# Performance work log

Measured on AMD Instinct MI355X. Metric: run time of the kernel, lower is better.

The kernel has to match this reference:

```python
import jax, jax.numpy as jnp
import numpy as np

B, S, D, H = 2, 2048, 1024, 16
DK = D // H
NEG = -1e9


def setup_inputs() -> dict:
    key = jax.random.key(0)
    ks = jax.random.split(key, 12)
    sc = 1.0 / np.sqrt(D)
    inp = {
        "query": jax.random.normal(ks[0], (B, S, D), jnp.float32),
        "key": jax.random.normal(ks[1], (B, S, D), jnp.float32),
        "value": jax.random.normal(ks[2], (B, S, D), jnp.float32),
        "mask": jnp.ones((B, 1, S), jnp.int32),
        "Wq": jax.random.normal(ks[3], (D, D), jnp.float32) * sc,
        "bq": jnp.zeros((D,), jnp.float32),
        "Wk": jax.random.normal(ks[4], (D, D), jnp.float32) * sc,
        "bk": jnp.zeros((D,), jnp.float32),
        "Wv": jax.random.normal(ks[5], (D, D), jnp.float32) * sc,
        "bv": jnp.zeros((D,), jnp.float32),
        "Wo": jax.random.normal(ks[6], (D, D), jnp.float32) * sc,
        "bo": jnp.zeros((D,), jnp.float32),
    }
    return inp


def reference(query, key, value, mask, Wq, bq, Wk, bk, Wv, bv, Wo, bo):
    # projections + split heads: [B,S,D] -> [B,H,S,DK]
    def proj(x, W, b):
        return (x @ W + b).reshape(B, S, H, DK).transpose(0, 2, 1, 3)

    q = proj(query, Wq, bq)
    k = proj(key, Wk, bk)
    v = proj(value, Wv, bv)

    scores = jnp.einsum("bhqd,bhkd->bhqk", q, k) / jnp.sqrt(jnp.float32(DK))
    # mask: [B,1,S] -> unsqueeze head dim -> [B,1,1,S], broadcast over heads & queries
    m = mask[:, None, :, :]  # [B,1,1,S]
    scores = jnp.where(m == 0, NEG, scores)
    p_attn = jax.nn.softmax(scores, axis=-1)  # dropout p=0 (eval)
    x = jnp.einsum("bhqk,bhkd->bhqd", p_attn, v)
    x = x.transpose(0, 2, 1, 3).reshape(B, S, D)
    return x @ Wo + bo
```

## Files before the change

### kernel.cpp

```cpp
#include <hip/hip_runtime.h>
#include <stdint.h>

typedef unsigned short u16;
typedef __bf16 bf16x8 __attribute__((ext_vector_type(8), may_alias));
typedef unsigned short u16x8 __attribute__((ext_vector_type(8), may_alias));
typedef unsigned short u16x4 __attribute__((ext_vector_type(4), may_alias));
typedef float f32x4 __attribute__((ext_vector_type(4)));
typedef float f32x16 __attribute__((ext_vector_type(16)));

__device__ __forceinline__ u16 f2bf(float f) {
    union { float f; uint32_t i; } v; v.f = f;
    return (u16)((v.i + 0x7FFFu + ((v.i >> 16) & 1u)) >> 16);
}

__device__ __forceinline__ float exp2_hw(float x) {
#if __has_builtin(__builtin_amdgcn_exp2f)
    return __builtin_amdgcn_exp2f(x);
#else
    float r; asm("v_exp_f32 %0, %1" : "=v"(r) : "v"(x)); return r;
#endif
}

__device__ __forceinline__ uint32_t cvt_pk_bf16(float a, float b) {
    uint32_t r;
    asm("v_cvt_pk_bf16_f32 %0, %1, %2" : "=v"(r) : "v"(a), "v"(b));
    return r;
}

__device__ __forceinline__ void gld_lds16(const u16* g, u16* l) {
    __builtin_amdgcn_global_load_lds(
        (const __attribute__((address_space(1))) unsigned int*)g,
        (__attribute__((address_space(3))) unsigned int*)l, 16, 0, 0);
}

__global__ __launch_bounds__(256) void cvt_all(
    const float* __restrict__ s0, const float* __restrict__ s1, const float* __restrict__ s2,
    const float* __restrict__ w0, const float* __restrict__ w1,
    const float* __restrict__ w2, const float* __restrict__ w3,
    u16* __restrict__ d0, u16* __restrict__ d1, u16* __restrict__ d2,
    u16* __restrict__ t0, u16* __restrict__ t1,
    u16* __restrict__ t2, u16* __restrict__ t3)
{
    __shared__ float L[64][65];
    const int z = blockIdx.z;
    const int tid = threadIdx.x;
    if (z < 3) {
        const float* s = (z == 0) ? s0 : (z == 1) ? s1 : s2;
        u16*         d = (z == 0) ? d0 : (z == 1) ? d1 : d2;
        const size_t base = ((size_t)blockIdx.x * 256 + tid) * 16;
        #pragma unroll
        for (int p = 0; p < 2; ++p) {
            float4 a = *reinterpret_cast<const float4*>(s + base + p * 8);
            float4 b = *reinterpret_cast<const float4*>(s + base + p * 8 + 4);
            u16x8 o;
            o[0] = f2bf(a.x); o[1] = f2bf(a.y); o[2] = f2bf(a.z); o[3] = f2bf(a.w);
            o[4] = f2bf(b.x); o[5] = f2bf(b.y); o[6] = f2bf(b.z); o[7] = f2bf(b.w);
            *reinterpret_cast<u16x8*>(d + base + p * 8) = o;
        }
    } else {
        if (blockIdx.x >= 256) return;
        const int zi = z - 3;
        const float* w = (zi == 0) ? w0 : (zi == 1) ? w1 : (zi == 2) ? w2 : w3;
        u16*         t = (zi == 0) ? t0 : (zi == 1) ? t1 : (zi == 2) ? t2 : t3;
        const int k0 = (blockIdx.x & 15) * 64, n0 = (blockIdx.x >> 4) * 64;
        const int rr = tid >> 6, cc = tid & 63;
        #pragma unroll
        for (int p = 0; p < 16; ++p)
            L[p * 4 + rr][cc] = w[(size_t)(k0 + p * 4 + rr) * 1024 + n0 + cc];
        __syncthreads();
        #pragma unroll
        for (int p = 0; p < 16; ++p)
            t[(size_t)(n0 + p * 4 + rr) * 1024 + k0 + cc] = f2bf(L[cc][p * 4 + rr]);
    }
}

__global__ __launch_bounds__(256) void gemm_bt(
    const u16* __restrict__ A0, const u16* __restrict__ A1, const u16* __restrict__ A2,
    const u16* __restrict__ B0, const u16* __restrict__ B1, const u16* __restrict__ B2,
    const float* __restrict__ c0, const float* __restrict__ c1, const float* __restrict__ c2,
    void* __restrict__ d0, void* __restrict__ d1, void* __restrict__ d2,
    int mode_override)
{
    __shared__ u16 As[128 * 32];
    __shared__ u16 Bs[128 * 32];

    const int z = blockIdx.z;
    const u16* A = (z == 0) ? A0 : (z == 1) ? A1 : A2;
    const u16* BT = (z == 0) ? B0 : (z == 1) ? B1 : B2;
    const float* bias = (z == 0) ? c0 : (z == 1) ? c1 : c2;
    void* dst = (z == 0) ? d0 : (z == 1) ? d1 : d2;
    const int mode = (mode_override >= 0) ? mode_override : ((z == 2) ? 2 : 0);

    const int tid  = threadIdx.x;
    const int wave = tid >> 6, lane = tid & 63;
    const int quad = lane >> 4, l15 = lane & 15;
    const int row0 = blockIdx.x * 128, col0 = blockIdx.y * 128;
    const int wrow = (wave >> 1) * 64, wcol = (wave & 1) * 64;

    f32x4 acc[4][4] = {};

    for (int k0 = 0; k0 < 1024; k0 += 32) {
        __syncthreads();
        #pragma unroll
        for (int j = 0; j < 2; ++j) {
            const int idx = j * 256 + tid;
            const int r = idx >> 2, kc = (idx & 3) * 8;
            gld_lds16(A  + (size_t)(row0 + r) * 1024 + k0 + kc,
                      &As[(size_t)(j * 256 + wave * 64) * 8]);
            gld_lds16(BT + (size_t)(col0 + r) * 1024 + k0 + kc,
                      &Bs[(size_t)(j * 256 + wave * 64) * 8]);
        }
        __syncthreads();

        bf16x8 a[4], b[4];
        #pragma unroll
        for (int i = 0; i < 4; ++i)
            a[i] = *reinterpret_cast<const bf16x8*>(&As[(wrow + i * 16 + l15) * 32 + quad * 8]);
        #pragma unroll
        for (int j = 0; j < 4; ++j)
            b[j] = *reinterpret_cast<const bf16x8*>(&Bs[(wcol + j * 16 + l15) * 32 + quad * 8]);
        #pragma unroll
        for (int i = 0; i < 4; ++i)
            #pragma unroll
            for (int j = 0; j < 4; ++j)
                acc[i][j] = __builtin_amdgcn_mfma_f32_16x16x32_bf16(a[i], b[j], acc[i][j], 0, 0, 0);
    }

    const float emul = (mode == 0 && z == 0 && mode_override < 0) ? 0.18033688011112042f : 1.0f;

    #pragma unroll
    for (int i = 0; i < 4; ++i) {
        #pragma unroll
        for (int j = 0; j < 4; ++j) {
            const int gc  = col0 + wcol + j * 16 + l15;
            const float bv = bias[gc];
            const int gr0 = row0 + wrow + i * 16 + quad * 4;
            if (mode == 3) {
                float* df = (float*)dst;
                #pragma unroll
                for (int r = 0; r < 4; ++r)
                    df[(size_t)(gr0 + r) * 1024 + gc] = acc[i][j][r] + bv;
            } else if (mode == 2) {
                u16* dp = (u16*)dst;
                const int b = gr0 >> 11, s = gr0 & 2047;
                const int h = gc >> 6,  dk = gc & 63;
                u16x4 pk;
                pk[0] = f2bf(acc[i][j][0] + bv);
                pk[1] = f2bf(acc[i][j][1] + bv);
                pk[2] = f2bf(acc[i][j][2] + bv);
                pk[3] = f2bf(acc[i][j][3] + bv);
                *reinterpret_cast<u16x4*>(dp + ((size_t)((b * 16 + h) * 64 + dk)) * 2048 + s) = pk;
            } else {
                u16* dp = (u16*)dst;
                #pragma unroll
                for (int r = 0; r < 4; ++r) {
                    const int gr = gr0 + r;
                    const int b = gr >> 11, s = gr & 2047;
                    const int h = gc >> 6, dk = gc & 63;
                    dp[((size_t)((b * 16 + h) * 2048 + s)) * 64 + dk] = f2bf((acc[i][j][r] + bv) * emul);
                }
            }
        }
    }
}

__global__ __launch_bounds__(256) void attn_fused(
    const u16* __restrict__ Qb, const u16* __restrict__ Kb,
    const u16* __restrict__ Vt, const int* __restrict__ mask,
    u16* __restrict__ ctx)
{
    __shared__ __align__(16) u16 Ks[8 * 512];
    __shared__ __align__(16) u16 Vs[8 * 512];
    __shared__ float Ls[4 * 32];

    const int tid  = threadIdx.x;
    const int w    = tid >> 6;
    const int lane = tid & 63;
    const int l31  = lane & 31;
    const int hi   = lane >> 5;

    const int id = blockIdx.x;
    const int sw = (id & 7) * 64 + (id >> 3);
    const int bh = sw >> 4;
    const int q0 = (sw & 15) * 128;
    const int b  = bh >> 4, h = bh & 15;

    const u16* Qp = Qb + (size_t)bh * 2048 * 64;
    const u16* Kp = Kb + (size_t)bh * 2048 * 64;
    const u16* Vp = Vt + (size_t)bh * 64 * 2048;
    const int* mp = mask + b * 2048;

    bf16x8 qf[4];
    {
        const u16* qrow = Qp + (size_t)(q0 + w * 32 + l31) * 64 + hi * 8;
        #pragma unroll
        for (int s = 0; s < 4; ++s)
            qf[s] = *reinterpret_cast<const bf16x8*>(qrow + s * 16);
    }

    const int scb = tid & 7, sr = tid >> 3;
    const u16* kg0 = Kp + (size_t)sr * 64 + scb * 8;
    const u16* vg0 = Vp + (size_t)sr * 2048 + scb * 8;
    u16* kd0 = &Ks[scb * 512 + ((sr     ) ^ scb) * 8];
    u16* kd1 = &Ks[scb * 512 + ((sr + 32) ^ scb) * 8];
    u16* vd0 = &Vs[scb * 512 + ((sr     ) ^ scb) * 8];
    u16* vd1 = &Vs[scb * 512 + ((sr + 32) ^ scb) * 8];

    u16x8 kr0 = *reinterpret_cast<const u16x8*>(kg0);
    u16x8 kr1 = *reinterpret_cast<const u16x8*>(kg0 + 32 * 64);
    u16x8 vr0 = *reinterpret_cast<const u16x8*>(vg0);
    u16x8 vr1 = *reinterpret_cast<const u16x8*>(vg0 + 32 * 2048);
    int mreg = mp[lane];

    f32x16 accO0 = {}, accO1 = {};
    float la0 = 0.f, la1 = 0.f, la2 = 0.f, la3 = 0.f;
    const int paddr = (lane ^ 32) << 2;

    for (int t = 0; t < 32; ++t) {
        const int kk = t * 64;
        __syncthreads();
        *reinterpret_cast<u16x8*>(kd0) = kr0;
        *reinterpret_cast<u16x8*>(kd1) = kr1;
        *reinterpret_cast<u16x8*>(vd0) = vr0;
        *reinterpret_cast<u16x8*>(vd1) = vr1;
        int mnext = 1;
        if (t < 31) {
            const u16* kg = kg0 + (size_t)(kk + 64) * 64;
            const u16* vg = vg0 + (kk + 64);
            kr0 = *reinterpret_cast<const u16x8*>(kg);
            kr1 = *reinterpret_cast<const u16x8*>(kg + 32 * 64);
            vr0 = *reinterpret_cast<const u16x8*>(vg);
            vr1 = *reinterpret_cast<const u16x8*>(vg + 32 * 2048);
            mnext = mp[kk + 64 + lane];
        }
        __syncthreads();

        const bool fullmask = (__ballot(mreg != 0) == ~0ull);
        mreg = mnext;

        #pragma unroll
        for (int hf = 0; hf < 2; ++hf) {
            f32x16 z = {};
            #pragma unroll
            for (int s = 0; s < 4; ++s) {
                const int cb = s * 2 + hi;
                const bf16x8 ak = *reinterpret_cast<const bf16x8*>(
                    &Ks[cb * 512 + ((hf * 32 + l31) ^ cb) * 8]);
                z = __builtin_amdgcn_mfma_f32_32x32x16_bf16(ak, qf[s], z, 0, 0, 0);
            }
            float p[16];
            #pragma unroll
            for (int r = 0; r < 16; ++r) p[r] = exp2_hw(z[r]);
            if (!fullmask) {
                #pragma unroll
                for (int r = 0; r < 16; ++r) {
                    const int kv = kk + hf * 32 + (r & 3) + 8 * (r >> 2) + 4 * hi;
                    if (mp[kv] == 0) p[r] = 0.f;
                }
            }
            la0 += p[0] + p[4] + p[8]  + p[12];
            la1 += p[1] + p[5] + p[9]  + p[13];
            la2 += p[2] + p[6] + p[10] + p[14];
            la3 += p[3] + p[7] + p[11] + p[15];

            const uint32_t wd0 = cvt_pk_bf16(p[0],  p[1]);
            const uint32_t wd1 = cvt_pk_bf16(p[2],  p[3]);
            const uint32_t wd2 = cvt_pk_bf16(p[4],  p[5]);
            const uint32_t wd3 = cvt_pk_bf16(p[6],  p[7]);
            const uint32_t wd4 = cvt_pk_bf16(p[8],  p[9]);
            const uint32_t wd5 = cvt_pk_bf16(p[10], p[11]);
            const uint32_t wd6 = cvt_pk_bf16(p[12], p[13]);
            const uint32_t wd7 = cvt_pk_bf16(p[14], p[15]);
            const uint32_t s0 = hi ? wd0 : wd2;
            const uint32_t s1 = hi ? wd1 : wd3;
            const uint32_t s2 = hi ? wd4 : wd6;
            const uint32_t s3 = hi ? wd5 : wd7;
            const uint32_t r0 = (uint32_t)__builtin_amdgcn_ds_bpermute(paddr, (int)s0);
            const uint32_t r1 = (uint32_t)__builtin_amdgcn_ds_bpermute(paddr, (int)s1);
            const uint32_t r2 = (uint32_t)__builtin_amdgcn_ds_bpermute(paddr, (int)s2);
            const uint32_t r3 = (uint32_t)__builtin_amdgcn_ds_bpermute(paddr, (int)s3);
            union { uint32_t u[4]; bf16x8 v; } A0, A1;
            A0.u[0] = hi ? r0  : wd0;
            A0.u[1] = hi ? r1  : wd1;
            A0.u[2] = hi ? wd2 : r0;
            A0.u[3] = hi ? wd3 : r1;
            A1.u[0] = hi ? r2  : wd4;
            A1.u[1] = hi ? r3  : wd5;
            A1.u[2] = hi ? wd6 : r2;
            A1.u[3] = hi ? wd7 : r3;

            const int ck0 = hf * 4 + hi;
            const int ck1 = hf * 4 + 2 + hi;
            const bf16x8 bv00 = *reinterpret_cast<const bf16x8*>(&Vs[ck0 * 512 + ((     l31) ^ ck0) * 8]);
            const bf16x8 bv01 = *reinterpret_cast<const bf16x8*>(&Vs[ck1 * 512 + ((     l31) ^ ck1) * 8]);
            const bf16x8 bv10 = *reinterpret_cast<const bf16x8*>(&Vs[ck0 * 512 + ((32 + l31) ^ ck0) * 8]);
            const bf16x8 bv11 = *reinterpret_cast<const bf16x8*>(&Vs[ck1 * 512 + ((32 + l31) ^ ck1) * 8]);
            accO0 = __builtin_amdgcn_mfma_f32_32x32x16_bf16(A0.v, bv00, accO0, 0, 0, 0);
            accO0 = __builtin_amdgcn_mfma_f32_32x32x16_bf16(A1.v, bv01, accO0, 0, 0, 0);
            accO1 = __builtin_amdgcn_mfma_f32_32x32x16_bf16(A0.v, bv10, accO1, 0, 0, 0);
            accO1 = __builtin_amdgcn_mfma_f32_32x32x16_bf16(A1.v, bv11, accO1, 0, 0, 0);
        }
    }

    float l_acc = (la0 + la1) + (la2 + la3);
    l_acc += __shfl_xor(l_acc, 32);
    const float inv = 1.0f / l_acc;
    if (lane < 32) Ls[w * 32 + l31] = inv;
    __syncthreads();

    #pragma unroll
    for (int r = 0; r < 16; ++r) {
        const int qr = (r & 3) + 8 * (r >> 2) + 4 * hi;
        const float iv = Ls[w * 32 + qr];
        u16* row = ctx + (size_t)(b * 2048 + q0 + w * 32 + qr) * 1024 + h * 64;
        row[l31]      = f2bf(accO0[r] * iv);
        row[32 + l31] = f2bf(accO1[r] * iv);
    }
}

extern "C" void kernel_launch(void* const* d_in, const int* in_sizes, int n_in,
                              void* d_out, int out_size, void* d_ws, size_t ws_size,
                              hipStream_t stream) {
    const float* query = (const float*)d_in[0];
    const float* key   = (const float*)d_in[1];
    const float* value = (const float*)d_in[2];
    const int*   mask  = (const int*)d_in[3];
    const float* Wq = (const float*)d_in[4];
    const float* bq = (const float*)d_in[5];
    const float* Wk = (const float*)d_in[6];
    const float* bk = (const float*)d_in[7];
    const float* Wv = (const float*)d_in[8];
    const float* bv = (const float*)d_in[9];
    const float* Wo = (const float*)d_in[10];
    const float* bo = (const float*)d_in[11];
    float* out = (float*)d_out;

    u16* ws   = (u16*)d_ws;
    u16* Xq   = ws;
    u16* Xk   = ws + 4194304;
    u16* Xv   = ws + 8388608;
    u16* WqT  = ws + 12582912;
    u16* WkT  = ws + 13631488;
    u16* WvT  = ws + 14680064;
    u16* WoT  = ws + 15728640;
    u16* Qb   = ws + 16777216;
    u16* Kb   = ws + 20971520;
    u16* Vt   = ws + 25165824;
    u16* ctx  = Xq;

    dim3 blk(256);
    cvt_all<<<dim3(1024, 1, 7), blk, 0, stream>>>(query, key, value, Wq, Wk, Wv, Wo,
                                                  Xq, Xk, Xv, WqT, WkT, WvT, WoT);
    gemm_bt<<<dim3(32, 8, 3),  blk, 0, stream>>>(Xq, Xk, Xv, WqT, WkT, WvT,
                                                 bq, bk, bv, Qb, Kb, Vt, -1);
    attn_fused<<<dim3(512), blk, 0, stream>>>(Qb, Kb, Vt, mask, ctx);
    gemm_bt<<<dim3(32, 8, 1),  blk, 0, stream>>>(ctx, ctx, ctx, WoT, WoT, WoT,
                                                 bo, bo, bo, out, out, out, 3);
}
```

Before: 245.9 us.

## Split attention KV tiles across two wave groups with double-buffered LDS

The attention kernel now runs 512 threads per block. Waves are split into two groups that each process half of every 64-key tile, and their partial output accumulators and row sums are reduced through shared memory at the end. K/V tiles are double-buffered in LDS, so the next tile's store overlaps the current compute and only one barrier is needed per iteration instead of two. The aim is more waves in flight for latency hiding, at the cost of an extra cross-wave reduction, more LDS per block, and the register pressure that comes with launch_bounds(512,4).

After: 236.1 us. -4.0%, faster.

```diff
diff --git a/kernel.cpp b/kernel.cpp
--- a/kernel.cpp
+++ b/kernel.cpp
@@ -164,20 +164,20 @@
     }
 }
 
-__global__ __launch_bounds__(256) void attn_fused(
+__global__ __launch_bounds__(512, 4) void attn_fused(
     const u16* __restrict__ Qb, const u16* __restrict__ Kb,
     const u16* __restrict__ Vt, const int* __restrict__ mask,
     u16* __restrict__ ctx)
 {
-    __shared__ __align__(16) u16 Ks[8 * 512];
-    __shared__ __align__(16) u16 Vs[8 * 512];
-    __shared__ float Ls[4 * 32];
+    __shared__ __align__(16) u16 SMEM[16896];
 
     const int tid  = threadIdx.x;
     const int w    = tid >> 6;
     const int lane = tid & 63;
     const int l31  = lane & 31;
     const int hi   = lane >> 5;
+    const int qw   = w & 3;
+    const int kh   = w >> 2;
 
     const int id = blockIdx.x;
     const int sw = (id & 7) * 64 + (id >> 3);
@@ -192,7 +192,7 @@
 
     bf16x8 qf[4];
     {
-        const u16* qrow = Qp + (size_t)(q0 + w * 32 + l31) * 64 + hi * 8;
+        const u16* qrow = Qp + (size_t)(q0 + qw * 32 + l31) * 64 + hi * 8;
         #pragma unroll
         for (int s = 0; s < 4; ++s)
             qf[s] = *reinterpret_cast<const bf16x8*>(qrow + s * 16);
@@ -201,120 +201,130 @@
     const int scb = tid & 7, sr = tid >> 3;
     const u16* kg0 = Kp + (size_t)sr * 64 + scb * 8;
     const u16* vg0 = Vp + (size_t)sr * 2048 + scb * 8;
-    u16* kd0 = &Ks[scb * 512 + ((sr     ) ^ scb) * 8];
-    u16* kd1 = &Ks[scb * 512 + ((sr + 32) ^ scb) * 8];
-    u16* vd0 = &Vs[scb * 512 + ((sr     ) ^ scb) * 8];
-    u16* vd1 = &Vs[scb * 512 + ((sr + 32) ^ scb) * 8];
-
-    u16x8 kr0 = *reinterpret_cast<const u16x8*>(kg0);
-    u16x8 kr1 = *reinterpret_cast<const u16x8*>(kg0 + 32 * 64);
-    u16x8 vr0 = *reinterpret_cast<const u16x8*>(vg0);
-    u16x8 vr1 = *reinterpret_cast<const u16x8*>(vg0 + 32 * 2048);
+    const int dK = scb * 512 + (sr ^ scb) * 8;
+
+    {
+        u16x8 kr = *reinterpret_cast<const u16x8*>(kg0);
+        u16x8 vr = *reinterpret_cast<const u16x8*>(vg0);
+        *reinterpret_cast<u16x8*>(&SMEM[dK])        = kr;
+        *reinterpret_cast<u16x8*>(&SMEM[4096 + dK]) = vr;
+    }
     int mreg = mp[lane];
+    __syncthreads();
 
     f32x16 accO0 = {}, accO1 = {};
     float la0 = 0.f, la1 = 0.f, la2 = 0.f, la3 = 0.f;
     const int paddr = (lane ^ 32) << 2;
 
+    int cur = 0;
     for (int t = 0; t < 32; ++t) {
         const int kk = t * 64;
+        u16x8 krn, vrn; int mnext = 1;
+        if (t < 31) {
+            krn = *reinterpret_cast<const u16x8*>(kg0 + (size_t)(kk + 64) * 64);
+            vrn = *reinterpret_cast<const u16x8*>(vg0 + (kk + 64));
+            mnext = mp[kk + 64 + lane];
+        }
+        const u16* Kb_ = &SMEM[cur * 8192];
+        const u16* Vb_ = &SMEM[cur * 8192 + 4096];
+
+        const bool fullmask = (__ballot(mreg != 0) == ~0ull);
+
+        f32x16 z = {};
+        #pragma unroll
+        for (int s = 0; s < 4; ++s) {
+            const int cb = s * 2 + hi;
+            const bf16x8 ak = *reinterpret_cast<const bf16x8*>(
+                &Kb_[cb * 512 + (((kh * 32 + l31)) ^ cb) * 8]);
+            z = __builtin_amdgcn_mfma_f32_32x32x16_bf16(ak, qf[s], z, 0, 0, 0);
+        }
+        float p[16];
+        #pragma unroll
+        for (int r = 0; r < 16; ++r) p[r] = exp2_hw(z[r]);
+        if (!fullmask) {
+            #pragma unroll
+            for (int r = 0; r < 16; ++r) {
+                const int kv = kk + kh * 32 + (r & 3) + 8 * (r >> 2) + 4 * hi;
+                if (mp[kv] == 0) p[r] = 0.f;
+            }
+        }
+        la0 += p[0] + p[4] + p[8]  + p[12];
+        la1 += p[1] + p[5] + p[9]  + p[13];
+        la2 += p[2] + p[6] + p[10] + p[14];
+        la3 += p[3] + p[7] + p[11] + p[15];
+
+        const uint32_t wd0 = cvt_pk_bf16(p[0],  p[1]);
+        const uint32_t wd1 = cvt_pk_bf16(p[2],  p[3]);
+        const uint32_t wd2 = cvt_pk_bf16(p[4],  p[5]);
+        const uint32_t wd3 = cvt_pk_bf16(p[6],  p[7]);
+        const uint32_t wd4 = cvt_pk_bf16(p[8],  p[9]);
+        const uint32_t wd5 = cvt_pk_bf16(p[10], p[11]);
+        const uint32_t wd6 = cvt_pk_bf16(p[12], p[13]);
+        const uint32_t wd7 = cvt_pk_bf16(p[14], p[15]);
+        const uint32_t s0 = hi ? wd0 : wd2;
+        const uint32_t s1 = hi ? wd1 : wd3;
+        const uint32_t s2 = hi ? wd4 : wd6;
+        const uint32_t s3 = hi ? wd5 : wd7;
+        const uint32_t r0 = (uint32_t)__builtin_amdgcn_ds_bpermute(paddr, (int)s0);
+        const uint32_t r1 = (uint32_t)__builtin_amdgcn_ds_bpermute(paddr, (int)s1);
+        const uint32_t r2 = (uint32_t)__builtin_amdgcn_ds_bpermute(paddr, (int)s2);
+        const uint32_t r3 = (uint32_t)__builtin_amdgcn_ds_bpermute(paddr, (int)s3);
+        union { uint32_t u[4]; bf16x8 v; } A0, A1;
+        A0.u[0] = hi ? r0  : wd0;
+        A0.u[1] = hi ? r1  : wd1;
+        A0.u[2] = hi ? wd2 : r0;
+        A0.u[3] = hi ? wd3 : r1;
+        A1.u[0] = hi ? r2  : wd4;
+        A1.u[1] = hi ? r3  : wd5;
+        A1.u[2] = hi ? wd6 : r2;
+        A1.u[3] = hi ? wd7 : r3;
+
+        const int ck0 = kh * 4 + hi;
+        const int ck1 = kh * 4 + 2 + hi;
+        const bf16x8 bv00 = *reinterpret_cast<const bf16x8*>(&Vb_[ck0 * 512 + ((     l31) ^ ck0) * 8]);
+        const bf16x8 bv01 = *reinterpret_cast<const bf16x8*>(&Vb_[ck1 * 512 + ((     l31) ^ ck1) * 8]);
+        const bf16x8 bv10 = *reinterpret_cast<const bf16x8*>(&Vb_[ck0 * 512 + ((32 + l31) ^ ck0) * 8]);
+        const bf16x8 bv11 = *reinterpret_cast<const bf16x8*>(&Vb_[ck1 * 512 + ((32 + l31) ^ ck1) * 8]);
+        accO0 = __builtin_amdgcn_mfma_f32_32x32x16_bf16(A0.v, bv00, accO0, 0, 0, 0);
+        accO0 = __builtin_amdgcn_mfma_f32_32x32x16_bf16(A1.v, bv01, accO0, 0, 0, 0);
+        accO1 = __builtin_amdgcn_mfma_f32_32x32x16_bf16(A0.v, bv10, accO1, 0, 0, 0);
+        accO1 = __builtin_amdgcn_mfma_f32_32x32x16_bf16(A1.v, bv11, accO1, 0, 0, 0);
+
+        if (t < 31) {
+            const int nb = (cur ^ 1) * 8192;
+            *reinterpret_cast<u16x8*>(&SMEM[nb + dK])        = krn;
+            *reinterpret_cast<u16x8*>(&SMEM[nb + 4096 + dK]) = vrn;
+        }
         __syncthreads();
-        *reinterpret_cast<u16x8*>(kd0) = kr0;
-        *reinterpret_cast<u16x8*>(kd1) = kr1;
-        *reinterpret_cast<u16x8*>(vd0) = vr0;
-        *reinterpret_cast<u16x8*>(vd1) = vr1;
-        int mnext = 1;
-        if (t < 31) {
-            const u16* kg = kg0 + (size_t)(kk + 64) * 64;
-            const u16* vg = vg0 + (kk + 64);
-            kr0 = *reinterpret_cast<const u16x8*>(kg);
-            kr1 = *reinterpret_cast<const u16x8*>(kg + 32 * 64);
-            vr0 = *reinterpret_cast<const u16x8*>(vg);
-            vr1 = *reinterpret_cast<const u16x8*>(vg + 32 * 2048);
-            mnext = mp[kk + 64 + lane];
-        }
-        __syncthreads();
-
-        const bool fullmask = (__ballot(mreg != 0) == ~0ull);
+        cur ^= 1;
         mreg = mnext;
-
-        #pragma unroll
-        for (int hf = 0; hf < 2; ++hf) {
-            f32x16 z = {};
-            #pragma unroll
-            for (int s = 0; s < 4; ++s) {
-                const int cb = s * 2 + hi;
-                const bf16x8 ak = *reinterpret_cast<const bf16x8*>(
-                    &Ks[cb * 512 + ((hf * 32 + l31) ^ cb) * 8]);
-                z = __builtin_amdgcn_mfma_f32_32x32x16_bf16(ak, qf[s], z, 0, 0, 0);
-            }
-            float p[16];
-            #pragma unroll
-            for (int r = 0; r < 16; ++r) p[r] = exp2_hw(z[r]);
-            if (!fullmask) {
-                #pragma unroll
-                for (int r = 0; r < 16; ++r) {
-                    const int kv = kk + hf * 32 + (r & 3) + 8 * (r >> 2) + 4 * hi;
-                    if (mp[kv] == 0) p[r] = 0.f;
-                }
-            }
-            la0 += p[0] + p[4] + p[8]  + p[12];
-            la1 += p[1] + p[5] + p[9]  + p[13];
-            la2 += p[2] + p[6] + p[10] + p[14];
-            la3 += p[3] + p[7] + p[11] + p[15];
-
-            const uint32_t wd0 = cvt_pk_bf16(p[0],  p[1]);
-            const uint32_t wd1 = cvt_pk_bf16(p[2],  p[3]);
-            const uint32_t wd2 = cvt_pk_bf16(p[4],  p[5]);
-            const uint32_t wd3 = cvt_pk_bf16(p[6],  p[7]);
-            const uint32_t wd4 = cvt_pk_bf16(p[8],  p[9]);
-            const uint32_t wd5 = cvt_pk_bf16(p[10], p[11]);
-            const uint32_t wd6 = cvt_pk_bf16(p[12], p[13]);
-            const uint32_t wd7 = cvt_pk_bf16(p[14], p[15]);
-            const uint32_t s0 = hi ? wd0 : wd2;
-            const uint32_t s1 = hi ? wd1 : wd3;
-            const uint32_t s2 = hi ? wd4 : wd6;
-            const uint32_t s3 = hi ? wd5 : wd7;
-            const uint32_t r0 = (uint32_t)__builtin_amdgcn_ds_bpermute(paddr, (int)s0);
-            const uint32_t r1 = (uint32_t)__builtin_amdgcn_ds_bpermute(paddr, (int)s1);
-            const uint32_t r2 = (uint32_t)__builtin_amdgcn_ds_bpermute(paddr, (int)s2);
-            const uint32_t r3 = (uint32_t)__builtin_amdgcn_ds_bpermute(paddr, (int)s3);
-            union { uint32_t u[4]; bf16x8 v; } A0, A1;
-            A0.u[0] = hi ? r0  : wd0;
-            A0.u[1] = hi ? r1  : wd1;
-            A0.u[2] = hi ? wd2 : r0;
-            A0.u[3] = hi ? wd3 : r1;
-            A1.u[0] = hi ? r2  : wd4;
-            A1.u[1] = hi ? r3  : wd5;
-            A1.u[2] = hi ? wd6 : r2;
-            A1.u[3] = hi ? wd7 : r3;
-
-            const int ck0 = hf * 4 + hi;
-            const int ck1 = hf * 4 + 2 + hi;
-            const bf16x8 bv00 = *reinterpret_cast<const bf16x8*>(&Vs[ck0 * 512 + ((     l31) ^ ck0) * 8]);
-            const bf16x8 bv01 = *reinterpret_cast<const bf16x8*>(&Vs[ck1 * 512 + ((     l31) ^ ck1) * 8]);
-            const bf16x8 bv10 = *reinterpret_cast<const bf16x8*>(&Vs[ck0 * 512 + ((32 + l31) ^ ck0) * 8]);
-            const bf16x8 bv11 = *reinterpret_cast<const bf16x8*>(&Vs[ck1 * 512 + ((32 + l31) ^ ck1) * 8]);
-            accO0 = __builtin_amdgcn_mfma_f32_32x32x16_bf16(A0.v, bv00, accO0, 0, 0, 0);
-            accO0 = __builtin_amdgcn_mfma_f32_32x32x16_bf16(A1.v, bv01, accO0, 0, 0, 0);
-            accO1 = __builtin_amdgcn_mfma_f32_32x32x16_bf16(A0.v, bv10, accO1, 0, 0, 0);
-            accO1 = __builtin_amdgcn_mfma_f32_32x32x16_bf16(A1.v, bv11, accO1, 0, 0, 0);
-        }
-    }
-
-    float l_acc = (la0 + la1) + (la2 + la3);
-    l_acc += __shfl_xor(l_acc, 32);
-    const float inv = 1.0f / l_acc;
-    if (lane < 32) Ls[w * 32 + l31] = inv;
+    }
+
+    float l_part = (la0 + la1) + (la2 + la3);
+    l_part += __shfl_xor(l_part, 32);
+    float* F = (float*)SMEM;
+    if (kh) {
+        #pragma unroll
+        for (int r = 0; r < 16; ++r) F[qw * 1024 + r * 64 + lane] = accO0[r];
+        #pragma unroll
+        for (int r = 0; r < 16; ++r) F[4096 + qw * 1024 + r * 64 + lane] = accO1[r];
+        if (lane < 32) F[8192 + qw * 32 + l31] = l_part;
+    }
     __syncthreads();
-
-    #pragma unroll
-    for (int r = 0; r < 16; ++r) {
-        const int qr = (r & 3) + 8 * (r >> 2) + 4 * hi;
-        const float iv = Ls[w * 32 + qr];
-        u16* row = ctx + (size_t)(b * 2048 + q0 + w * 32 + qr) * 1024 + h * 64;
-        row[l31]      = f2bf(accO0[r] * iv);
-        row[32 + l31] = f2bf(accO1[r] * iv);
+    if (!kh && lane < 32)
+        F[8320 + qw * 32 + l31] = 1.0f / (l_part + F[8192 + qw * 32 + l31]);
+    __syncthreads();
+    if (!kh) {
+        #pragma unroll
+        for (int r = 0; r < 16; ++r) {
+            const int qr = (r & 3) + 8 * (r >> 2) + 4 * hi;
+            const float iv = F[8320 + qw * 32 + qr];
+            const float o0 = accO0[r] + F[qw * 1024 + r * 64 + lane];
+            const float o1 = accO1[r] + F[4096 + qw * 1024 + r * 64 + lane];
+            u16* row = ctx + (size_t)(b * 2048 + q0 + qw * 32 + qr) * 1024 + h * 64;
+            row[l31]      = f2bf(o0 * iv);
+            row[32 + l31] = f2bf(o1 * iv);
+        }
     }
 }
 
@@ -353,7 +363,7 @@
                                                   Xq, Xk, Xv, WqT, WkT, WvT, WoT);
     gemm_bt<<<dim3(32, 8, 3),  blk, 0, stream>>>(Xq, Xk, Xv, WqT, WkT, WvT,
                                                  bq, bk, bv, Qb, Kb, Vt, -1);
-    attn_fused<<<dim3(512), blk, 0, stream>>>(Qb, Kb, Vt, mask, ctx);
+    attn_fused<<<dim3(512), dim3(512), 0, stream>>>(Qb, Kb, Vt, mask, ctx);
     gemm_bt<<<dim3(32, 8, 1),  blk, 0, stream>>>(ctx, ctx, ctx, WoT, WoT, WoT,
                                                  bo, bo, bo, out, out, out, 3);
 }
```
